# Kernel tuning notes

Measured on AMD Instinct MI355X. Metric: run time of the kernel, lower is better.

## Reference

```python
import jax, jax.numpy as jnp
import numpy as np

LOG2 = float(np.log(2.0))

def shifted_softplus(x):
    # softplus(x) - log(2), numerically stable
    return jax.nn.softplus(x) - LOG2

def setup_inputs() -> dict:
    key = jax.random.key(0)
    ks = jax.random.split(key, 6)
    N, E, D, C = 50000, 800000, 64, 64
    in_features = 2 * D + D  # 192
    h = jax.random.normal(ks[0], (N, D), dtype=jnp.float32)
    edge_attr = jax.random.normal(ks[1], (E, D), dtype=jnp.float32)
    edge_index = jax.random.randint(ks[2], (2, E), 0, N, dtype=jnp.int64)
    # Linear weights (stored transposed relative to torch: [in, out])
    W1 = jax.random.normal(ks[3], (in_features, 2 * C), dtype=jnp.float32) * (1.0 / np.sqrt(in_features))
    b1 = jnp.zeros((2 * C,), dtype=jnp.float32)
    W2 = jax.random.normal(ks[4], (2 * C, C), dtype=jnp.float32) * (1.0 / np.sqrt(2 * C))
    b2 = jnp.zeros((C,), dtype=jnp.float32)
    return {"h": h, "edge_attr": edge_attr, "edge_index": edge_index,
            "W1": W1, "b1": b1, "W2": W2, "b2": b2}

def reference(h, edge_attr, edge_index, W1, b1, W2, b2):
    h1 = h[edge_index[0, :]]                       # [E, D] gather
    h2 = h[edge_index[1, :]]                       # [E, D] gather
    concat = jnp.concatenate((h1, h2, edge_attr), axis=1)  # [E, 2D + De]
    x = shifted_softplus(concat @ W1 + b1)          # [E, 2C]
    x = x @ W2 + b2                                 # [E, C]
    return x
```

## Files before the change

### kernel.cpp

```cpp
#include <hip/hip_runtime.h>
#include <cstddef>
#include <cstdint>

typedef __attribute__((ext_vector_type(8))) short bf16x8;
typedef __attribute__((ext_vector_type(16))) float f32x16;

static constexpr float LN2 = 0.69314718055994530942f;
static constexpr float INV_LN2 = 1.44269504088896340736f;

__device__ __forceinline__ unsigned short f2bf(float f) {
  unsigned int u = __float_as_uint(f);
  u += 0x7fffu + ((u >> 16) & 1u);
  return (unsigned short)(u >> 16);
}

__device__ __forceinline__ unsigned int cvt_pk_bf16(float a, float b) {
  unsigned int r;
  asm("v_cvt_pk_bf16_f32 %0, %1, %2" : "=v"(r) : "v"(a), "v"(b));
  return r;
}

__device__ __forceinline__ float hw_exp2(float x) {
  float r;
  asm("v_exp_f32 %0, %1" : "=v"(r) : "v"(x));
  return r;
}
__device__ __forceinline__ float hw_log2(float x) {
  float r;
  asm("v_log_f32 %0, %1" : "=v"(r) : "v"(x));
  return r;
}

__device__ __forceinline__ float shsp(float x) {
  float t = hw_exp2(-fabsf(x) * INV_LN2);
  float l = hw_log2(1.0f + t);
  return fmaf(LN2, l, fmaxf(x, 0.0f) - LN2);
}

__device__ __forceinline__ void async_copy16(const void* g, void* l) {
  __builtin_amdgcn_global_load_lds(
      (const __attribute__((address_space(1))) void*)g,
      (__attribute__((address_space(3))) void*)l, 16, 0, 0);
}

#define WAITV(N) asm volatile("s_waitcnt vmcnt(" #N ")" ::: "memory")

__global__ void prep_h_kernel(const float* __restrict__ h,
                              unsigned short* __restrict__ hbf, int n4) {
  int i = blockIdx.x * 256 + threadIdx.x;
  if (i < n4) {
    float4 v = reinterpret_cast<const float4*>(h)[i];
    uint2 o;
    o.x = cvt_pk_bf16(v.x, v.y);
    o.y = cvt_pk_bf16(v.z, v.w);
    reinterpret_cast<uint2*>(hbf)[i] = o;
  }
}

__global__ void prep_w_kernel(const float* __restrict__ W1,
                              const float* __restrict__ W2,
                              unsigned short* __restrict__ Wp1,
                              unsigned short* __restrict__ Wp2) {
  int j = blockIdx.x * 256 + threadIdx.x;
  if (j < 48 * 64) {
    int f  = j / 64;
    int l  = j % 64;
    int kk = f >> 2;
    int mt = f & 3;
    int col = mt * 32 + (l & 31);
    int kb  = kk * 16 + (l >> 5) * 8;
    #pragma unroll
    for (int i = 0; i < 8; ++i)
      Wp1[(size_t)j * 8 + i] = f2bf(W1[(size_t)(kb + i) * 128 + col]);
  } else if (j < 48 * 64 + 16 * 64) {
    int jj = j - 48 * 64;
    int f  = jj / 64;
    int l  = jj % 64;
    int kk = f >> 1;
    int mt = f & 1;
    int oc = mt * 32 + (l & 31);
    int kb = kk * 16 + (l >> 5) * 8;
    #pragma unroll
    for (int i = 0; i < 8; ++i)
      Wp2[(size_t)jj * 8 + i] = f2bf(W2[(size_t)(kb + i) * 64 + oc]);
  }
}

__global__ __launch_bounds__(704, 1)
void edge_mlp_kernel(const float* __restrict__ ea,
                     const int* __restrict__ eidx,
                     const float* __restrict__ b1,
                     const float* __restrict__ b2,
                     const unsigned short* __restrict__ hbf,
                     const unsigned short* __restrict__ Wp1,
                     float* __restrict__ out,
                     int E, int ntiles) {
  __shared__ __align__(16) unsigned char LDS[156416];

  const int tid  = threadIdx.x;
  const int lane = tid & 63;
  const int w    = tid >> 6;
  const int lo   = lane & 31;
  const int hi   = lane >> 5;
  const int rsw  = lo & 7;
  const int l8   = lane >> 3;
  const int p    = lane & 7;

  unsigned char* W1L = LDS;
  unsigned char* W2L = LDS + 49152;
  unsigned char* HA0 = LDS + 65536 + w * 8192;
  float*         BL1 = reinterpret_cast<float*>(LDS + 155648);
  float*         BL2 = reinterpret_cast<float*>(LDS + 155648 + 512);

  #pragma unroll
  for (int j = 0; j < 6; ++j) {
    int ch = j * 704 + w * 64;
    if (ch < 4096)
      async_copy16(Wp1 + (size_t)(ch + lane) * 8, LDS + ch * 16);
  }
  if (tid < 32) {
    float4 v = reinterpret_cast<const float4*>(b1)[tid];
    reinterpret_cast<float4*>(BL1)[tid] = v;
  } else if (tid < 48) {
    float4 v = reinterpret_cast<const float4*>(b2)[tid - 32];
    reinterpret_cast<float4*>(BL2)[tid - 32] = v;
  }
  __syncthreads();

  const int gw     = blockIdx.x * 11 + w;
  const int nwaves = gridDim.x * 11;
  const int tmax   = ntiles - 1;

  float4 eareg[8];
  bf16x8 h2reg[4];
  int nodeN1 = 0;

#define IDX1(t) eidx[(size_t)(t) * 32 + lo]
#define IDX2(t) eidx[(size_t)E + (size_t)(t) * 32 + lo]

#define LOADEA(t) { \
  const float* eab_ = ea + (size_t)((t) * 32 + lo) * 64; \
  _Pragma("unroll") for (int j = 0; j < 4; ++j) { \
    eareg[2 * j]     = *reinterpret_cast<const float4*>(eab_ + j * 16 + hi * 8); \
    eareg[2 * j + 1] = *reinterpret_cast<const float4*>(eab_ + j * 16 + hi * 8 + 4); \
  } }

#define LOADH2(NODE2) { \
  const unsigned short* hb_ = hbf + (size_t)(NODE2) * 64; \
  _Pragma("unroll") for (int k2 = 0; k2 < 4; ++k2) \
    h2reg[k2] = *reinterpret_cast<const bf16x8*>(hb_ + (2 * k2 + hi) * 8); }

#define ISSUE_H1(NODE, HBASE) { \
  _Pragma("unroll") for (int it = 0; it < 4; ++it) { \
    int r_ = it * 8 + l8; \
    int c_ = p ^ (r_ & 7); \
    int nd_ = __shfl(NODE, r_, 64); \
    async_copy16(hbf + (size_t)nd_ * 64 + c_ * 8, (HBASE) + it * 1024); \
  } }

  int t = gw;
  if (t < ntiles) {
    int node2c = IDX2(t);
    int node1c = IDX1(t);
    LOADEA(t)
    LOADH2(node2c)
    ISSUE_H1(node1c, HA0)
    nodeN1 = IDX1(min(t + nwaves, tmax));
    WAITV(0);
  }

  int cur = 0;
  for (; t < ntiles; t += nwaves) {
    unsigned char* HAc = HA0 + cur * 4096;
    unsigned char* HAn = HA0 + (cur ^ 1) * 4096;
    const int eb  = t * 32;
    const int tn  = min(t + nwaves, tmax);
    const int tnn = min(t + 2 * nwaves, tmax);

    WAITV(22);

    ISSUE_H1(nodeN1, HAn)
    int node1new = IDX1(tnn);
    int node2new = IDX2(tn);

    f32x16 acc[4];
    #pragma unroll
    for (int m = 0; m < 4; ++m) acc[m] = (f32x16)0.0f;

    __builtin_amdgcn_s_setprio(1);
    #pragma unroll
    for (int kk = 0; kk < 12; ++kk) {
      bf16x8 bfr;
      if (kk < 4) {
        bfr = *reinterpret_cast<const bf16x8*>(
            HAc + lo * 128 + (((2 * kk + hi) ^ rsw) * 16));
      } else if (kk < 8) {
        bfr = h2reg[kk - 4];
      } else {
        float4 lo4 = eareg[(kk - 8) * 2];
        float4 hi4 = eareg[(kk - 8) * 2 + 1];
        union { bf16x8 v; unsigned u[4]; } tt;
        tt.u[0] = cvt_pk_bf16(lo4.x, lo4.y);
        tt.u[1] = cvt_pk_bf16(lo4.z, lo4.w);
        tt.u[2] = cvt_pk_bf16(hi4.x, hi4.y);
        tt.u[3] = cvt_pk_bf16(hi4.z, hi4.w);
        bfr = tt.v;
      }
      #pragma unroll
      for (int mt = 0; mt < 4; ++mt) {
        bf16x8 afr = *reinterpret_cast<const bf16x8*>(
            W1L + (size_t)(kk * 4 + mt) * 1024 + lane * 16);
        acc[mt] = __builtin_amdgcn_mfma_f32_32x32x16_bf16(afr, bfr, acc[mt], 0, 0, 0);
      }
    }
    __builtin_amdgcn_s_setprio(0);

    LOADEA(tn)
    LOADH2(node2new)

    unsigned u0[16], u1[16];
    #pragma unroll
    for (int c = 0; c < 16; ++c) {
      int mt = c >> 2, g = c & 3;
      float4 bb = *reinterpret_cast<const float4*>(BL1 + mt * 32 + g * 8 + hi * 4);
      float s0 = shsp(acc[mt][g * 4 + 0] + bb.x);
      float s1 = shsp(acc[mt][g * 4 + 1] + bb.y);
      float s2 = shsp(acc[mt][g * 4 + 2] + bb.z);
      float s3 = shsp(acc[mt][g * 4 + 3] + bb.w);
      u0[c] = cvt_pk_bf16(s0, s1);
      u1[c] = cvt_pk_bf16(s2, s3);
    }

    unsigned pa[8][4];
    #pragma unroll
    for (int kk = 0; kk < 8; ++kk) {
      unsigned x0 = u0[2 * kk], y0 = u0[2 * kk + 1];
      unsigned x1 = u1[2 * kk], y1 = u1[2 * kk + 1];
      unsigned s0 = hi ? x0 : y0;
      unsigned s1 = hi ? x1 : y1;
      unsigned t0 = (unsigned)__shfl_xor((int)s0, 32, 64);
      unsigned t1 = (unsigned)__shfl_xor((int)s1, 32, 64);
      pa[kk][0] = hi ? t0 : x0;
      pa[kk][1] = hi ? t1 : x1;
      pa[kk][2] = hi ? y0 : t0;
      pa[kk][3] = hi ? y1 : t1;
    }

    f32x16 acc2[2];
    #pragma unroll
    for (int m = 0; m < 2; ++m) acc2[m] = (f32x16)0.0f;

    __builtin_amdgcn_s_setprio(1);
    #pragma unroll
    for (int kk = 0; kk < 8; ++kk) {
      union { bf16x8 v; unsigned u[4]; } tt;
      tt.u[0] = pa[kk][0];
      tt.u[1] = pa[kk][1];
      tt.u[2] = pa[kk][2];
      tt.u[3] = pa[kk][3];
      #pragma unroll
      for (int mt = 0; mt < 2; ++mt) {
        bf16x8 afr = *reinterpret_cast<const bf16x8*>(
            W2L + (size_t)(kk * 2 + mt) * 1024 + lane * 16);
        acc2[mt] = __builtin_amdgcn_mfma_f32_32x32x16_bf16(afr, tt.v, acc2[mt], 0, 0, 0);
      }
    }
    __builtin_amdgcn_s_setprio(0);

    #pragma unroll
    for (int mt = 0; mt < 2; ++mt) {
      #pragma unroll
      for (int g = 0; g < 4; ++g) {
        float4 bb = *reinterpret_cast<const float4*>(BL2 + mt * 32 + g * 8 + hi * 4);
        float4 o;
        o.x = acc2[mt][g * 4 + 0] + bb.x;
        o.y = acc2[mt][g * 4 + 1] + bb.y;
        o.z = acc2[mt][g * 4 + 2] + bb.z;
        o.w = acc2[mt][g * 4 + 3] + bb.w;
        int c = g * 2 + hi;
        *reinterpret_cast<float4*>(HAc + lo * 128 + ((c ^ rsw) * 16)) = o;
      }
      #pragma unroll
      for (int it = 0; it < 4; ++it) {
        int r = it * 8 + l8;
        float4 v = *reinterpret_cast<const float4*>(HAc + r * 128 + p * 16);
        int c = p ^ (r & 7);
        *reinterpret_cast<float4*>(
            out + (size_t)(eb + r) * 64 + mt * 32 + c * 4) = v;
      }
    }

    nodeN1 = node1new;
    cur ^= 1;
  }
}

extern "C" void kernel_launch(void* const* d_in, const int* in_sizes, int n_in,
                              void* d_out, int out_size, void* d_ws, size_t ws_size,
                              hipStream_t stream) {
  const float* h  = (const float*)d_in[0];
  const float* ea = (const float*)d_in[1];
  const int*  idx = (const int*)d_in[2];
  const float* W1 = (const float*)d_in[3];
  const float* b1 = (const float*)d_in[4];
  const float* W2 = (const float*)d_in[5];
  const float* b2 = (const float*)d_in[6];
  float* out = (float*)d_out;

  const int N = in_sizes[0] / 64;
  const int E = in_sizes[1] / 64;

  unsigned short* hbf = (unsigned short*)d_ws;
  size_t off1 = (size_t)N * 64 * 2;
  unsigned short* Wp1 = (unsigned short*)((char*)d_ws + off1);
  unsigned short* Wp2 = Wp1 + 24576;

  int n4 = (N * 64) / 4;
  prep_h_kernel<<<(n4 + 255) / 256, 256, 0, stream>>>(h, hbf, n4);
  prep_w_kernel<<<16, 256, 0, stream>>>(W1, W2, Wp1, Wp2);

  int ntiles = E / 32;
  edge_mlp_kernel<<<256, 704, 0, stream>>>(ea, idx, b1, b2, hbf, Wp1,
                                           out, E, ntiles);
}
```

Measured before the change: 121.6 us.

## Single-buffer H1 staging, store output directly, and raise to 12 waves per block

Replaces the per-wave double-buffered LDS staging of gathered h1 rows with a single buffer, issued after the first GEMM instead of one tile ahead. The output is now written straight from the accumulators to global memory, no longer transposed through LDS for coalesced stores. The freed LDS lets the block grow from 11 to 12 waves. The aim is more parallel waves to hide latency, at the cost of a shorter h1 prefetch distance and less coalesced output writes.

Measured after the change: 150.0 us. +23.4%, slower.

```diff
diff --git a/kernel.cpp b/kernel.cpp
--- a/kernel.cpp
+++ b/kernel.cpp
@@ -86,7 +86,7 @@
   }
 }
 
-__global__ __launch_bounds__(704, 1)
+__global__ __launch_bounds__(768, 1)
 void edge_mlp_kernel(const float* __restrict__ ea,
                      const int* __restrict__ eidx,
                      const float* __restrict__ b1,
@@ -95,7 +95,7 @@
                      const unsigned short* __restrict__ Wp1,
                      float* __restrict__ out,
                      int E, int ntiles) {
-  __shared__ __align__(16) unsigned char LDS[156416];
+  __shared__ __align__(16) unsigned char LDS[115456];
 
   const int tid  = threadIdx.x;
   const int lane = tid & 63;
@@ -108,13 +108,13 @@
 
   unsigned char* W1L = LDS;
   unsigned char* W2L = LDS + 49152;
-  unsigned char* HA0 = LDS + 65536 + w * 8192;
-  float*         BL1 = reinterpret_cast<float*>(LDS + 155648);
-  float*         BL2 = reinterpret_cast<float*>(LDS + 155648 + 512);
+  unsigned char* HAw = LDS + 65536 + w * 4096;
+  float*         BL1 = reinterpret_cast<float*>(LDS + 114688);
+  float*         BL2 = reinterpret_cast<float*>(LDS + 114688 + 512);
 
   #pragma unroll
   for (int j = 0; j < 6; ++j) {
-    int ch = j * 704 + w * 64;
+    int ch = j * 768 + w * 64;
     if (ch < 4096)
       async_copy16(Wp1 + (size_t)(ch + lane) * 8, LDS + ch * 16);
   }
@@ -127,13 +127,12 @@
   }
   __syncthreads();
 
-  const int gw     = blockIdx.x * 11 + w;
-  const int nwaves = gridDim.x * 11;
+  const int gw     = blockIdx.x * 12 + w;
+  const int nwaves = gridDim.x * 12;
   const int tmax   = ntiles - 1;
 
   float4 eareg[8];
   bf16x8 h2reg[4];
-  int nodeN1 = 0;
 
 #define IDX1(t) eidx[(size_t)(t) * 32 + lo]
 #define IDX2(t) eidx[(size_t)E + (size_t)(t) * 32 + lo]
@@ -150,38 +149,32 @@
   _Pragma("unroll") for (int k2 = 0; k2 < 4; ++k2) \
     h2reg[k2] = *reinterpret_cast<const bf16x8*>(hb_ + (2 * k2 + hi) * 8); }
 
-#define ISSUE_H1(NODE, HBASE) { \
+#define ISSUE_H1(NODE) { \
   _Pragma("unroll") for (int it = 0; it < 4; ++it) { \
     int r_ = it * 8 + l8; \
     int c_ = p ^ (r_ & 7); \
     int nd_ = __shfl(NODE, r_, 64); \
-    async_copy16(hbf + (size_t)nd_ * 64 + c_ * 8, (HBASE) + it * 1024); \
+    async_copy16(hbf + (size_t)nd_ * 64 + c_ * 8, HAw + it * 1024); \
   } }
 
   int t = gw;
   if (t < ntiles) {
+    int node1c = IDX1(t);
     int node2c = IDX2(t);
-    int node1c = IDX1(t);
     LOADEA(t)
     LOADH2(node2c)
-    ISSUE_H1(node1c, HA0)
-    nodeN1 = IDX1(min(t + nwaves, tmax));
+    ISSUE_H1(node1c)
     WAITV(0);
   }
 
-  int cur = 0;
   for (; t < ntiles; t += nwaves) {
-    unsigned char* HAc = HA0 + cur * 4096;
-    unsigned char* HAn = HA0 + (cur ^ 1) * 4096;
-    const int eb  = t * 32;
-    const int tn  = min(t + nwaves, tmax);
-    const int tnn = min(t + 2 * nwaves, tmax);
-
-    WAITV(22);
-
-    ISSUE_H1(nodeN1, HAn)
-    int node1new = IDX1(tnn);
-    int node2new = IDX2(tn);
+    const int eb = t * 32;
+    const int tn = min(t + nwaves, tmax);
+
+    WAITV(20);
+
+    int node1n = IDX1(tn);
+    int node2n = IDX2(tn);
 
     f32x16 acc[4];
     #pragma unroll
@@ -193,7 +186,7 @@
       bf16x8 bfr;
       if (kk < 4) {
         bfr = *reinterpret_cast<const bf16x8*>(
-            HAc + lo * 128 + (((2 * kk + hi) ^ rsw) * 16));
+            HAw + lo * 128 + (((2 * kk + hi) ^ rsw) * 16));
       } else if (kk < 8) {
         bfr = h2reg[kk - 4];
       } else {
@@ -215,8 +208,9 @@
     }
     __builtin_amdgcn_s_setprio(0);
 
+    ISSUE_H1(node1n)
     LOADEA(tn)
-    LOADH2(node2new)
+    LOADH2(node2n)
 
     unsigned u0[16], u1[16];
     #pragma unroll
@@ -277,21 +271,10 @@
         o.y = acc2[mt][g * 4 + 1] + bb.y;
         o.z = acc2[mt][g * 4 + 2] + bb.z;
         o.w = acc2[mt][g * 4 + 3] + bb.w;
-        int c = g * 2 + hi;
-        *reinterpret_cast<float4*>(HAc + lo * 128 + ((c ^ rsw) * 16)) = o;
+        *reinterpret_cast<float4*>(
+            out + (size_t)(eb + lo) * 64 + mt * 32 + g * 8 + hi * 4) = o;
       }
-      #pragma unroll
-      for (int it = 0; it < 4; ++it) {
-        int r = it * 8 + l8;
-        float4 v = *reinterpret_cast<const float4*>(HAc + r * 128 + p * 16);
-        int c = p ^ (r & 7);
-        *reinterpret_cast<float4*>(
-            out + (size_t)(eb + r) * 64 + mt * 32 + c * 4) = v;
-      }
-    }
-
-    nodeN1 = node1new;
-    cur ^= 1;
+    }
   }
 }
 
@@ -320,6 +303,6 @@
   prep_w_kernel<<<16, 256, 0, stream>>>(W1, W2, Wp1, Wp2);
 
   int ntiles = E / 32;
-  edge_mlp_kernel<<<256, 704, 0, stream>>>(ea, idx, b1, b2, hbf, Wp1,
+  edge_mlp_kernel<<<256, 768, 0, stream>>>(ea, idx, b1, b2, hbf, Wp1,
                                            out, E, ntiles);
 }
```
